# Kernel optimization log

Measured on AMD Instinct MI355X. Metric: run time of the kernel, lower is better.

The kernel has to match this reference:

```python
import jax, jax.numpy as jnp
import numpy as np


def setup_inputs() -> dict:
    key = jax.random.key(0)
    ks = jax.random.split(key, 6)
    B = 65536
    x = jax.random.normal(ks[0], (B, 784), dtype=jnp.float32)
    conv_w = jax.random.normal(ks[1], (3, 3), dtype=jnp.float32)
    fc1_w = jax.random.normal(ks[2], (100, 676), dtype=jnp.float32) * (1.0 / np.sqrt(676))
    fc1_b = jax.random.normal(ks[3], (100,), dtype=jnp.float32) * 0.01
    fc2_w = jax.random.normal(ks[4], (10, 100), dtype=jnp.float32) * (1.0 / np.sqrt(100))
    fc2_b = jax.random.normal(ks[5], (10,), dtype=jnp.float32) * 0.01
    return {"x": x, "conv_w": conv_w, "fc1_w": fc1_w, "fc1_b": fc1_b, "fc2_w": fc2_w, "fc2_b": fc2_b}


def reference(x, conv_w, fc1_w, fc1_b, fc2_w, fc2_b):
    B = x.shape[0]
    img = x.reshape(B, 1, 28, 28)  # NCHW, single channel
    kern = conv_w.reshape(1, 1, 3, 3)  # OIHW
    # 'valid' cross-correlation, matching the slicing-based Convolve()
    conv = jax.lax.conv_general_dilated(
        img, kern, window_strides=(1, 1), padding='VALID',
        dimension_numbers=('NCHW', 'OIHW', 'NCHW'))  # [B,1,26,26]
    h = conv.reshape(B, 26 * 26)
    h = jax.nn.relu(h @ fc1_w.T + fc1_b)
    out = h @ fc2_w.T + fc2_b
    return out
```

## Files before the change

kernel.cpp:

```cpp
#include <hip/hip_runtime.h>


typedef short  s16x8 __attribute__((ext_vector_type(8)));
typedef float  f32x4 __attribute__((ext_vector_type(4)));

#define BM   32
#define XP   808
#define HSTR 132
#define NT   8
#define KC   25

__device__ __forceinline__ unsigned short f2bf_rtne(float f) {
    unsigned int u = __builtin_bit_cast(unsigned int, f);
    u = (u + 0x7fffu + ((u >> 16) & 1u)) >> 16;
    return (unsigned short)u;
}

extern "C" __global__ void __launch_bounds__(256)
prep_w1eff(const float* __restrict__ W1, const float* __restrict__ cw9,
           const float* __restrict__ b1, unsigned short* __restrict__ bw)
{
    int id = blockIdx.x * 256 + threadIdx.x;
    if (id >= NT * KC * 64) return;
    int lane = id & 63;
    int kc   = (id >> 6) % KC;
    int t    = id / (KC * 64);
    int n    = t * 16 + (lane & 15);
    int k0   = kc * 32 + (lane >> 4) * 8;

    float cw[9];
#pragma unroll
    for (int i = 0; i < 9; ++i) cw[i] = cw9[i];

    unsigned short v[8];
#pragma unroll
    for (int j = 0; j < 8; ++j) {
        int k = k0 + j;
        float f = 0.f;
        if (n < 100) {
            if (k < 784) {
                int i = k / 28, jj = k % 28;
                for (int dr = 0; dr < 3; ++dr)
                    for (int dc = 0; dc < 3; ++dc) {
                        int a = i - dr, b = jj - dc;
                        if (a >= 0 && a < 26 && b >= 0 && b < 26)
                            f = fmaf(W1[(size_t)n * 676 + a * 26 + b],
                                     cw[dr * 3 + dc], f);
                    }
            } else if (k == 784) {
                f = b1[n];
            }
        }
        v[j] = f2bf_rtne(f);
    }
    *(uint4*)(bw + (size_t)id * 8) = *(const uint4*)v;
}

extern "C" __global__ void __launch_bounds__(256, 3)
digit_gemm(const float* __restrict__ x,
           const unsigned short* __restrict__ bw,
           const float* __restrict__ W2,
           const float* __restrict__ b2,
           float* __restrict__ out)
{
    __shared__ __align__(16) unsigned char smem[BM * XP * 2];
    unsigned short* xbuf = (unsigned short*)smem;
    float*          hbuf = (float*)smem;

    const int tid  = threadIdx.x;
    const int lane = tid & 63;
    const int wv   = tid >> 6;
    const int q    = lane >> 4;
    const int mn   = lane & 15;
    const int m0   = blockIdx.x * BM;

    {
        int mi = tid >> 3, u = tid & 7;
        *(unsigned int*)(xbuf + mi * XP + 784 + u * 2) = (u == 0) ? 0x3F80u : 0u;
    }

    const float4* xg = (const float4*)(x + (size_t)m0 * 784);
    for (int rr = 0; rr < 3; ++rr) {
        float4 v[8];
#pragma unroll
        for (int i = 0; i < 8; ++i)
            v[i] = xg[tid + 256 * (rr * 8 + i)];
#pragma unroll
        for (int i = 0; i < 8; ++i) {
            int g  = tid + 256 * (rr * 8 + i);
            int mi = g / 196, c4 = g - mi * 196;
            unsigned int ax = __builtin_bit_cast(unsigned int, v[i].x) + 0x8000u;
            unsigned int ay = __builtin_bit_cast(unsigned int, v[i].y) + 0x8000u;
            unsigned int az = __builtin_bit_cast(unsigned int, v[i].z) + 0x8000u;
            unsigned int aw = __builtin_bit_cast(unsigned int, v[i].w) + 0x8000u;
            uint2 w;
            w.x = (ax >> 16) | (ay & 0xffff0000u);
            w.y = (az >> 16) | (aw & 0xffff0000u);
            *(uint2*)(xbuf + mi * XP + c4 * 4) = w;
        }
    }
    if (tid < 128) {
        int g  = 6144 + tid;
        float4 vv = xg[g];
        int mi = g / 196, c4 = g - mi * 196;
        unsigned int ax = __builtin_bit_cast(unsigned int, vv.x) + 0x8000u;
        unsigned int ay = __builtin_bit_cast(unsigned int, vv.y) + 0x8000u;
        unsigned int az = __builtin_bit_cast(unsigned int, vv.z) + 0x8000u;
        unsigned int aw = __builtin_bit_cast(unsigned int, vv.w) + 0x8000u;
        uint2 w;
        w.x = (ax >> 16) | (ay & 0xffff0000u);
        w.y = (az >> 16) | (aw & 0xffff0000u);
        *(uint2*)(xbuf + mi * XP + c4 * 4) = w;
    }
    __syncthreads();

    f32x4 acc00, acc01, acc10, acc11;
#pragma unroll
    for (int i = 0; i < 4; ++i) { acc00[i]=0.f; acc01[i]=0.f; acc10[i]=0.f; acc11[i]=0.f; }

    const unsigned short* arow0 = xbuf + mn * XP + q * 8;
    const unsigned short* arow1 = xbuf + (16 + mn) * XP + q * 8;
    const uint4* bwv = (const uint4*)bw;
    const int t0 = wv, t1 = wv + 4;

    uint4 a0 = *(const uint4*)(arow0);
    uint4 a1 = *(const uint4*)(arow1);
    uint4 b0 = bwv[(t0 * KC) * 64 + lane];
    uint4 b1 = bwv[(t1 * KC) * 64 + lane];
    for (int kc = 0; kc < KC; ++kc) {
        int kn = (kc + 1 < KC) ? kc + 1 : kc;
        uint4 na0 = *(const uint4*)(arow0 + kn * 32);
        uint4 na1 = *(const uint4*)(arow1 + kn * 32);
        uint4 nb0 = bwv[(t0 * KC + kn) * 64 + lane];
        uint4 nb1 = bwv[(t1 * KC + kn) * 64 + lane];
        s16x8 av0 = __builtin_bit_cast(s16x8, a0), av1 = __builtin_bit_cast(s16x8, a1);
        s16x8 bv0 = __builtin_bit_cast(s16x8, b0), bv1 = __builtin_bit_cast(s16x8, b1);
        acc00 = __builtin_amdgcn_mfma_f32_16x16x32_bf16(av0, bv0, acc00, 0, 0, 0);
        acc01 = __builtin_amdgcn_mfma_f32_16x16x32_bf16(av0, bv1, acc01, 0, 0, 0);
        acc10 = __builtin_amdgcn_mfma_f32_16x16x32_bf16(av1, bv0, acc10, 0, 0, 0);
        acc11 = __builtin_amdgcn_mfma_f32_16x16x32_bf16(av1, bv1, acc11, 0, 0, 0);
        a0 = na0; a1 = na1; b0 = nb0; b1 = nb1;
    }
    __syncthreads();

#pragma unroll
    for (int r = 0; r < 4; ++r) {
        int row = q * 4 + r;
        float v;
        v = acc00[r]; v = v > 0.f ? v : 0.f; hbuf[ row       * HSTR + t0 * 16 + mn] = v;
        v = acc01[r]; v = v > 0.f ? v : 0.f; hbuf[ row       * HSTR + t1 * 16 + mn] = v;
        v = acc10[r]; v = v > 0.f ? v : 0.f; hbuf[(row + 16) * HSTR + t0 * 16 + mn] = v;
        v = acc11[r]; v = v > 0.f ? v : 0.f; hbuf[(row + 16) * HSTR + t1 * 16 + mn] = v;
    }
    __syncthreads();

    for (int p = tid; p < BM * 10; p += 256) {
        int mi = p / 10, o = p - mi * 10;
        const float4* hv = (const float4*)(hbuf + mi * HSTR);
        const float4* w2 = (const float4*)(W2 + (size_t)o * 100);
        float s = b2[o];
#pragma unroll
        for (int g = 0; g < 25; ++g) {
            float4 h4 = hv[g], w4 = w2[g];
            s += h4.x*w4.x + h4.y*w4.y + h4.z*w4.z + h4.w*w4.w;
        }
        out[(size_t)(m0 + mi) * 10 + o] = s;
    }
}

extern "C" void kernel_launch(void* const* d_in, const int* in_sizes, int n_in,
                              void* d_out, int out_size, void* d_ws, size_t ws_size,
                              hipStream_t stream) {
    const float* x  = (const float*)d_in[0];
    const float* cw = (const float*)d_in[1];
    const float* W1 = (const float*)d_in[2];
    const float* b1 = (const float*)d_in[3];
    const float* W2 = (const float*)d_in[4];
    const float* b2 = (const float*)d_in[5];
    float* out = (float*)d_out;
    unsigned short* bw = (unsigned short*)d_ws;

    const int B = in_sizes[0] / 784;

    hipLaunchKernelGGL(prep_w1eff, dim3((NT * KC * 64 + 255) / 256), dim3(256),
                       0, stream, W1, cw, b1, bw);
    hipLaunchKernelGGL(digit_gemm, dim3(B / BM), dim3(256), 0, stream,
                       x, bw, W2, b2, out);
}
```

Before: 320.2 us.

## Feed MFMA directly from global x, dropping LDS staging of inputs

Each wave now loads its own 16 rows of x straight from global memory with a one-step register prefetch. It converts them to bf16 in registers and computes 7 of the N tiles (112 columns, only the 100 valid ones are kept). This removes the block-wide LDS staging pass and its barrier, and the bias column is injected via a constant fragment on the last K chunk. The block tile grows to 64 rows and occupancy is raised to 4 waves per SIMD. In exchange, each wave issues strided global reads and 7 B-fragment loads per K step, and uses more accumulator registers.

Result: slower. 340.3 us (+6.3%).

```diff
diff --git a/kernel.cpp b/kernel.cpp
--- a/kernel.cpp
+++ b/kernel.cpp
@@ -4,10 +4,10 @@
 typedef short  s16x8 __attribute__((ext_vector_type(8)));
 typedef float  f32x4 __attribute__((ext_vector_type(4)));
 
-#define BM   32
-#define XP   808
-#define HSTR 132
+#define BM   64
+#define HSTR 116
 #define NT   8
+#define NTL  7
 #define KC   25
 
 __device__ __forceinline__ unsigned short f2bf_rtne(float f) {
@@ -56,16 +56,31 @@
     *(uint4*)(bw + (size_t)id * 8) = *(const uint4*)v;
 }
 
-extern "C" __global__ void __launch_bounds__(256, 3)
+__device__ __forceinline__ s16x8 cvt8(float4 a, float4 b) {
+    unsigned int ax = __builtin_bit_cast(unsigned int, a.x) + 0x8000u;
+    unsigned int ay = __builtin_bit_cast(unsigned int, a.y) + 0x8000u;
+    unsigned int az = __builtin_bit_cast(unsigned int, a.z) + 0x8000u;
+    unsigned int aw = __builtin_bit_cast(unsigned int, a.w) + 0x8000u;
+    unsigned int bx = __builtin_bit_cast(unsigned int, b.x) + 0x8000u;
+    unsigned int by = __builtin_bit_cast(unsigned int, b.y) + 0x8000u;
+    unsigned int bz = __builtin_bit_cast(unsigned int, b.z) + 0x8000u;
+    unsigned int bw_ = __builtin_bit_cast(unsigned int, b.w) + 0x8000u;
+    uint4 u;
+    u.x = (ax >> 16) | (ay & 0xffff0000u);
+    u.y = (az >> 16) | (aw & 0xffff0000u);
+    u.z = (bx >> 16) | (by & 0xffff0000u);
+    u.w = (bz >> 16) | (bw_ & 0xffff0000u);
+    return __builtin_bit_cast(s16x8, u);
+}
+
+extern "C" __global__ void __launch_bounds__(256, 4)
 digit_gemm(const float* __restrict__ x,
            const unsigned short* __restrict__ bw,
            const float* __restrict__ W2,
            const float* __restrict__ b2,
            float* __restrict__ out)
 {
-    __shared__ __align__(16) unsigned char smem[BM * XP * 2];
-    unsigned short* xbuf = (unsigned short*)smem;
-    float*          hbuf = (float*)smem;
+    __shared__ __align__(16) float hbuf[BM * HSTR];
 
     const int tid  = threadIdx.x;
     const int lane = tid & 63;
@@ -74,84 +89,57 @@
     const int mn   = lane & 15;
     const int m0   = blockIdx.x * BM;
 
-    {
-        int mi = tid >> 3, u = tid & 7;
-        *(unsigned int*)(xbuf + mi * XP + 784 + u * 2) = (u == 0) ? 0x3F80u : 0u;
+    const float* arow = x + (size_t)(m0 + wv * 16 + mn) * 784;
+    const uint4* bwv  = (const uint4*)bw;
+
+    f32x4 acc[NTL];
+#pragma unroll
+    for (int t = 0; t < NTL; ++t) {
+        acc[t][0] = 0.f; acc[t][1] = 0.f; acc[t][2] = 0.f; acc[t][3] = 0.f;
     }
 
-    const float4* xg = (const float4*)(x + (size_t)m0 * 784);
-    for (int rr = 0; rr < 3; ++rr) {
-        float4 v[8];
+    float4 c0, c1;
+    {
+        const float* p = arow + q * 8;
+        c0 = *(const float4*)p; c1 = *(const float4*)(p + 4);
+    }
+
+    for (int kc = 0; kc < KC; ++kc) {
+        int kn  = (kc + 1 < KC) ? kc + 1 : KC - 1;
+        int off = kn * 32 + q * 8;
+        const float* p = arow + (off < 784 ? off : 0);
+        float4 n0 = *(const float4*)p;
+        float4 n1 = *(const float4*)(p + 4);
+
+        uint4 bvv[NTL];
 #pragma unroll
-        for (int i = 0; i < 8; ++i)
-            v[i] = xg[tid + 256 * (rr * 8 + i)];
-#pragma unroll
-        for (int i = 0; i < 8; ++i) {
-            int g  = tid + 256 * (rr * 8 + i);
-            int mi = g / 196, c4 = g - mi * 196;
-            unsigned int ax = __builtin_bit_cast(unsigned int, v[i].x) + 0x8000u;
-            unsigned int ay = __builtin_bit_cast(unsigned int, v[i].y) + 0x8000u;
-            unsigned int az = __builtin_bit_cast(unsigned int, v[i].z) + 0x8000u;
-            unsigned int aw = __builtin_bit_cast(unsigned int, v[i].w) + 0x8000u;
-            uint2 w;
-            w.x = (ax >> 16) | (ay & 0xffff0000u);
-            w.y = (az >> 16) | (aw & 0xffff0000u);
-            *(uint2*)(xbuf + mi * XP + c4 * 4) = w;
+        for (int t = 0; t < NTL; ++t)
+            bvv[t] = bwv[(size_t)(t * KC + kc) * 64 + lane];
+
+        s16x8 av = cvt8(c0, c1);
+        if (kc == KC - 1) {
+            if (q >= 2) {
+                uint4 z; z.x = (q == 2) ? 0x3F80u : 0u; z.y = 0u; z.z = 0u; z.w = 0u;
+                av = __builtin_bit_cast(s16x8, z);
+            }
         }
-    }
-    if (tid < 128) {
-        int g  = 6144 + tid;
-        float4 vv = xg[g];
-        int mi = g / 196, c4 = g - mi * 196;
-        unsigned int ax = __builtin_bit_cast(unsigned int, vv.x) + 0x8000u;
-        unsigned int ay = __builtin_bit_cast(unsigned int, vv.y) + 0x8000u;
-        unsigned int az = __builtin_bit_cast(unsigned int, vv.z) + 0x8000u;
-        unsigned int aw = __builtin_bit_cast(unsigned int, vv.w) + 0x8000u;
-        uint2 w;
-        w.x = (ax >> 16) | (ay & 0xffff0000u);
-        w.y = (az >> 16) | (aw & 0xffff0000u);
-        *(uint2*)(xbuf + mi * XP + c4 * 4) = w;
-    }
-    __syncthreads();
-
-    f32x4 acc00, acc01, acc10, acc11;
-#pragma unroll
-    for (int i = 0; i < 4; ++i) { acc00[i]=0.f; acc01[i]=0.f; acc10[i]=0.f; acc11[i]=0.f; }
-
-    const unsigned short* arow0 = xbuf + mn * XP + q * 8;
-    const unsigned short* arow1 = xbuf + (16 + mn) * XP + q * 8;
-    const uint4* bwv = (const uint4*)bw;
-    const int t0 = wv, t1 = wv + 4;
-
-    uint4 a0 = *(const uint4*)(arow0);
-    uint4 a1 = *(const uint4*)(arow1);
-    uint4 b0 = bwv[(t0 * KC) * 64 + lane];
-    uint4 b1 = bwv[(t1 * KC) * 64 + lane];
-    for (int kc = 0; kc < KC; ++kc) {
-        int kn = (kc + 1 < KC) ? kc + 1 : kc;
-        uint4 na0 = *(const uint4*)(arow0 + kn * 32);
-        uint4 na1 = *(const uint4*)(arow1 + kn * 32);
-        uint4 nb0 = bwv[(t0 * KC + kn) * 64 + lane];
-        uint4 nb1 = bwv[(t1 * KC + kn) * 64 + lane];
-        s16x8 av0 = __builtin_bit_cast(s16x8, a0), av1 = __builtin_bit_cast(s16x8, a1);
-        s16x8 bv0 = __builtin_bit_cast(s16x8, b0), bv1 = __builtin_bit_cast(s16x8, b1);
-        acc00 = __builtin_amdgcn_mfma_f32_16x16x32_bf16(av0, bv0, acc00, 0, 0, 0);
-        acc01 = __builtin_amdgcn_mfma_f32_16x16x32_bf16(av0, bv1, acc01, 0, 0, 0);
-        acc10 = __builtin_amdgcn_mfma_f32_16x16x32_bf16(av1, bv0, acc10, 0, 0, 0);
-        acc11 = __builtin_amdgcn_mfma_f32_16x16x32_bf16(av1, bv1, acc11, 0, 0, 0);
-        a0 = na0; a1 = na1; b0 = nb0; b1 = nb1;
-    }
-    __syncthreads();
 
 #pragma unroll
-    for (int r = 0; r < 4; ++r) {
-        int row = q * 4 + r;
-        float v;
-        v = acc00[r]; v = v > 0.f ? v : 0.f; hbuf[ row       * HSTR + t0 * 16 + mn] = v;
-        v = acc01[r]; v = v > 0.f ? v : 0.f; hbuf[ row       * HSTR + t1 * 16 + mn] = v;
-        v = acc10[r]; v = v > 0.f ? v : 0.f; hbuf[(row + 16) * HSTR + t0 * 16 + mn] = v;
-        v = acc11[r]; v = v > 0.f ? v : 0.f; hbuf[(row + 16) * HSTR + t1 * 16 + mn] = v;
+        for (int t = 0; t < NTL; ++t)
+            acc[t] = __builtin_amdgcn_mfma_f32_16x16x32_bf16(
+                av, __builtin_bit_cast(s16x8, bvv[t]), acc[t], 0, 0, 0);
+
+        c0 = n0; c1 = n1;
     }
+
+#pragma unroll
+    for (int t = 0; t < NTL; ++t)
+#pragma unroll
+        for (int r = 0; r < 4; ++r) {
+            float v = acc[t][r];
+            v = v > 0.f ? v : 0.f;
+            hbuf[(wv * 16 + q * 4 + r) * HSTR + t * 16 + mn] = v;
+        }
     __syncthreads();
 
     for (int p = tid; p < BM * 10; p += 256) {
@@ -162,7 +150,7 @@
 #pragma unroll
         for (int g = 0; g < 25; ++g) {
             float4 h4 = hv[g], w4 = w2[g];
-            s += h4.x*w4.x + h4.y*w4.y + h4.z*w4.z + h4.w*w4.w;
+            s += h4.x * w4.x + h4.y * w4.y + h4.z * w4.z + h4.w * w4.w;
         }
         out[(size_t)(m0 + mi) * 10 + o] = s;
     }
```
